# Kernel optimization log

Hardware: AMD Instinct MI355X
Metric: run time of the kernel (lower is better)

## Reference

```python
import jax, jax.numpy as jnp
import numpy as np
from jax import lax

N = 40       # num_users
K = 20       # num_channels
F = 3        # num_features (conv length dim)
SS = K * N   # state_size = 800
B = 16384


def _conv1d(x, w, b):
    # x: [B, C_in, L], w: [C_out, C_in, 3], SAME padding (pad=1)
    y = lax.conv_general_dilated(x, w, window_strides=(1,), padding=[(1, 1)],
                                 dimension_numbers=('NCH', 'OIH', 'NCH'))
    return y + b[None, :, None]


def _get_mask(state):
    # state: [B, SS, F]; status feature is index 2 (== -1 since F=3)
    visited = state[:, :, 2] != 0.0                      # [B, SS]
    vm = visited.reshape(B, K, N)                        # [B, K, N] (flat idx = chan*N + user)
    user_any = vm.any(axis=1)                            # [B, N]: user visited on any channel
    chan_full = vm.sum(axis=2) >= 2                      # [B, K]: channel has >=2 users
    mask = visited \
        | jnp.broadcast_to(user_any[:, None, :], (B, K, N)).reshape(B, SS) \
        | jnp.broadcast_to(chan_full[:, :, None], (B, K, N)).reshape(B, SS)
    return mask


def setup_inputs() -> dict:
    key = jax.random.key(0)
    ks = jax.random.split(key, 12)
    state = jax.random.normal(ks[0], (B, SS, F), jnp.float32)
    keep = jax.random.bernoulli(ks[1], 0.02, (B, SS)).astype(jnp.float32)
    state = state.at[:, :, 2].multiply(keep)
    s = 0.02
    w1 = jax.random.normal(ks[2], (128, SS, 3), jnp.float32) * s
    b1 = jnp.zeros((128,), jnp.float32)
    w2 = jax.random.normal(ks[3], (256, 128, 3), jnp.float32) * s
    b2 = jnp.zeros((256,), jnp.float32)
    w3 = jax.random.normal(ks[4], (128, 256, 3), jnp.float32) * s
    b3 = jnp.zeros((128,), jnp.float32)
    wl1 = jax.random.normal(ks[5], (64 * F, 128 * F), jnp.float32) * s   # [192, 384]
    bl1 = jnp.zeros((64 * F,), jnp.float32)
    wl2 = jax.random.normal(ks[6], (SS, 64 * F), jnp.float32) * s        # [800, 192]
    bl2 = jnp.zeros((SS,), jnp.float32)
    return {"state": state, "w1": w1, "b1": b1, "w2": w2, "b2": b2,
            "w3": w3, "b3": b3, "wl1": wl1, "bl1": bl1, "wl2": wl2, "bl2": bl2}


def reference(state, w1, b1, w2, b2, w3, b3, wl1, bl1, wl2, bl2):
    mask = _get_mask(state)
    x = jax.nn.relu(_conv1d(state, w1, b1))   # [B,128,3]
    x = jax.nn.relu(_conv1d(x, w2, b2))       # [B,256,3]
    x = jax.nn.relu(_conv1d(x, w3, b3))       # [B,128,3]
    x = x.reshape(B, -1)                      # [B,384]
    x = jax.nn.relu(x @ wl1.T + bl1)          # [B,192]
    out = x @ wl2.T + bl2                     # [B,800]
    return jnp.where(mask, -jnp.inf, out)
```

## Files before the change

kernel.cpp:

```cpp
#include <hip/hip_runtime.h>
#include <cstdint>
#include <cstddef>
#include <math.h>

typedef short bf16x8 __attribute__((ext_vector_type(8)));
typedef float f32x4 __attribute__((ext_vector_type(4)));
typedef unsigned long long u64;

#define NEG_HUGE (-3.0e38f)

__device__ __forceinline__ ushort f2bf(float x) {
    union { float f; uint32_t u; } a; a.f = x;
    uint32_t r = a.u + 0x7FFF + ((a.u >> 16) & 1);
    return (ushort)(r >> 16);
}

__device__ __forceinline__ void gload_lds16(const void* g, void* l) {
    __builtin_amdgcn_global_load_lds(
        (const __attribute__((address_space(1))) uint32_t*)g,
        (__attribute__((address_space(3))) uint32_t*)l, 16, 0, 0);
}

#define SCHED() __builtin_amdgcn_sched_barrier(0)
#define SBAR() do { SCHED(); __builtin_amdgcn_s_barrier(); SCHED(); } while (0)

__global__ void prep_conv_T(const float* __restrict__ w, ushort* __restrict__ WT,
                            int Cin, int Cout, int Nrows, int Kpad) {
    int idx = blockIdx.x * 256 + threadIdx.x;
    if (idx >= Nrows * Kpad) return;
    int n = idx / Kpad, k = idx - n * Kpad;
    float val = 0.f;
    if (k < Cin * 3) {
        int co = n / 3, l = n % 3, ci = k / 3, lx = k % 3;
        int t = lx - l + 1;
        if (t >= 0 && t < 3) val = w[(co * Cin + ci) * 3 + t];
    }
    WT[idx] = f2bf(val);
}

__global__ void prep_lin_T(const float* __restrict__ wl, ushort* __restrict__ WT,
                           int K, int Nreal, int Npad) {
    int idx = blockIdx.x * 256 + threadIdx.x;
    if (idx >= Npad * K) return;
    int n = idx / K, k = idx - n * K;
    WT[idx] = (n < Nreal) ? f2bf(wl[n * K + k]) : (ushort)0;
}

__global__ __launch_bounds__(512, 2)
void conv1_kernel(const float* __restrict__ state, const ushort* __restrict__ W1T,
                  const float* __restrict__ b1, ushort* __restrict__ X1g,
                  uint32_t* __restrict__ maskg)
{
    extern __shared__ char lds[];
    char* BF0 = lds;
    char* BF1 = lds + 8192;
    char* Wb0 = lds + 16384;
    char* Wb1 = lds + 65536;
    uint32_t* maskw = (uint32_t*)(lds + 114688);

    const int tid = threadIdx.x, lane = tid & 63, wid = tid >> 6;
    const int m0 = blockIdx.x * 64;
    const int ml = lane & 15, kq = lane >> 4;
    const int mbase = (wid >> 2) * 32;
    const int wn0 = (wid & 3) * 96;

    const int srow = tid >> 3, seg = tid & 7;
    const float* sbase = state + (size_t)(m0 + srow) * 2400 + seg * 8;

    f32x4 acc[6][2];
    #pragma unroll
    for (int f = 0; f < 6; ++f)
        #pragma unroll
        for (int mi = 0; mi < 2; ++mi) acc[f][mi] = (f32x4){0.f, 0.f, 0.f, 0.f};

    auto loadS = [&](float4 (&sv)[2], int c) {
        int kb = c * 64 + seg * 8;
        if (kb < 2400) {
            sv[0] = *(const float4*)(sbase + c * 64);
            sv[1] = *(const float4*)(sbase + c * 64 + 4);
        } else {
            sv[0] = (float4){0.f, 0.f, 0.f, 0.f};
            sv[1] = (float4){0.f, 0.f, 0.f, 0.f};
        }
    };
    auto stage_write = [&](float4 (&sv)[2], int c, char* dst) {
        float fv[8] = {sv[0].x, sv[0].y, sv[0].z, sv[0].w,
                       sv[1].x, sv[1].y, sv[1].z, sv[1].w};
        bf16x8 h;
        #pragma unroll
        for (int j = 0; j < 8; ++j) h[j] = (short)f2bf(fv[j]);
        *(bf16x8*)(dst + srow * 128 + ((seg * 16) ^ ((srow & 7) << 4))) = h;
        int kbase = c * 64 + seg * 8;
        int kmod = kbase % 3;
        uint32_t* mrow = &maskw[srow * 25];
        #define MCHK(J) { if (fv[J] != 0.0f) { int a = (kbase + (J)) / 3; \
                          atomicOr(&mrow[a >> 5], 1u << (a & 31)); } }
        if (kmod == 0)      { MCHK(2) MCHK(5) }
        else if (kmod == 1) { MCHK(1) MCHK(4) MCHK(7) }
        else                { MCHK(0) MCHK(3) MCHK(6) }
        #undef MCHK
    };
    auto loadW = [&](int c, char* dst) {
        #pragma unroll
        for (int i = 0; i < 6; ++i) {
            int s = i * 512 + tid;
            int r = s >> 3, o8 = s & 7;
            gload_lds16(W1T + (size_t)r * 2432 + c * 64 + ((o8 ^ (r & 7)) * 8),
                        dst + s * 16);
        }
    };
    auto mfmaC = [&](const char* wb, const char* sb) {
        #pragma unroll
        for (int ks = 0; ks < 2; ++ks) {
            bf16x8 af[6], bv[2];
            #pragma unroll
            for (int f = 0; f < 6; ++f) {
                int n = wn0 + f * 16 + ml;
                af[f] = *(const bf16x8*)(wb + n * 128 + (((ks * 4 + kq) * 16) ^ ((n & 7) << 4)));
            }
            #pragma unroll
            for (int mi = 0; mi < 2; ++mi) {
                int m = mbase + mi * 16 + ml;
                bv[mi] = *(const bf16x8*)(sb + m * 128 + (((ks * 4 + kq) * 16) ^ ((m & 7) << 4)));
            }
            #pragma unroll
            for (int f = 0; f < 6; ++f)
                #pragma unroll
                for (int mi = 0; mi < 2; ++mi)
                    acc[f][mi] = __builtin_amdgcn_mfma_f32_16x16x32_bf16(af[f], bv[mi], acc[f][mi], 0, 0, 0);
        }
    };

    for (int i = tid; i < 64 * 25; i += 512) maskw[i] = 0;
    float4 svA[2], svB[2];
    loadS(svA, 0);
    loadS(svB, 1);
    loadW(0, Wb0);
    asm volatile("s_waitcnt lgkmcnt(0)" ::: "memory");
    SBAR();

    #define BODY(SV, C, SB, WBC, WBN) do {                                   \
        stage_write(SV, (C), SB);                                            \
        loadS(SV, ((C) + 2 > 37) ? 37 : (C) + 2);                            \
        SCHED();                                                             \
        asm volatile("s_waitcnt lgkmcnt(0)" ::: "memory");                   \
        SBAR();                                                              \
        loadW(((C) + 1 > 37) ? 37 : (C) + 1, WBN);                           \
        SCHED();                                                             \
        asm volatile("s_waitcnt vmcnt(8)" ::: "memory");                     \
        SBAR();                                                              \
        mfmaC(WBC, SB);                                                      \
    } while (0)

    #pragma unroll 1
    for (int p = 0; p < 19; ++p) {
        BODY(svA, 2 * p,     BF0, Wb0, Wb1);
        BODY(svB, 2 * p + 1, BF1, Wb1, Wb0);
    }
    #undef BODY

    asm volatile("s_waitcnt vmcnt(0) lgkmcnt(0)" ::: "memory");
    SBAR();

    {
        const int nq4 = (lane >> 4) * 4;
        #pragma unroll
        for (int f = 0; f < 6; ++f) {
            int n4 = wn0 + f * 16 + nq4;
            float bv0 = b1[n4 / 3], bv1 = b1[(n4 + 1) / 3];
            float bv2 = b1[(n4 + 2) / 3], bv3 = b1[(n4 + 3) / 3];
            #pragma unroll
            for (int mi = 0; mi < 2; ++mi) {
                int m = mbase + mi * 16 + ml;
                ushort4 o;
                o.x = f2bf(fmaxf(acc[f][mi][0] + bv0, 0.f));
                o.y = f2bf(fmaxf(acc[f][mi][1] + bv1, 0.f));
                o.z = f2bf(fmaxf(acc[f][mi][2] + bv2, 0.f));
                o.w = f2bf(fmaxf(acc[f][mi][3] + bv3, 0.f));
                *(ushort4*)(X1g + (size_t)(m0 + m) * 384 + n4) = o;
            }
        }
    }

    if (tid < 64) {
        uint32_t* mw = &maskw[tid * 25];
        const u64 M40 = (1ull << 40) - 1;
        u64 ua = 0; uint32_t cf = 0;
        #pragma unroll
        for (int g = 0; g < 5; ++g) {
            uint32_t w0 = mw[5*g], w1 = mw[5*g+1], w2 = mw[5*g+2], w3 = mw[5*g+3], w4 = mw[5*g+4];
            u64 c0 = ( (u64)w0        | ((u64)w1 << 32)) & M40;
            u64 c1 = (((u64)w1 >> 8)  | ((u64)w2 << 24)) & M40;
            u64 c2 = (((u64)w2 >> 16) | ((u64)w3 << 16)) & M40;
            u64 c3 = (((u64)w3 >> 24) | ((u64)w4 << 8))  & M40;
            ua |= c0 | c1 | c2 | c3;
            if (__popcll(c0) >= 2) cf |= 1u << (4*g);
            if (__popcll(c1) >= 2) cf |= 1u << (4*g+1);
            if (__popcll(c2) >= 2) cf |= 1u << (4*g+2);
            if (__popcll(c3) >= 2) cf |= 1u << (4*g+3);
        }
        uint32_t* mg = maskg + (size_t)(m0 + tid) * 25;
        #pragma unroll
        for (int g = 0; g < 5; ++g) {
            uint32_t w0 = mw[5*g], w1 = mw[5*g+1], w2 = mw[5*g+2], w3 = mw[5*g+3], w4 = mw[5*g+4];
            u64 c0 = ( (u64)w0        | ((u64)w1 << 32)) & M40;
            u64 c1 = (((u64)w1 >> 8)  | ((u64)w2 << 24)) & M40;
            u64 c2 = (((u64)w2 >> 16) | ((u64)w3 << 16)) & M40;
            u64 c3 = (((u64)w3 >> 24) | ((u64)w4 << 8))  & M40;
            u64 m0v = c0 | ua | (((cf >> (4*g))     & 1u) ? M40 : 0ull);
            u64 m1v = c1 | ua | (((cf >> (4*g + 1)) & 1u) ? M40 : 0ull);
            u64 m2v = c2 | ua | (((cf >> (4*g + 2)) & 1u) ? M40 : 0ull);
            u64 m3v = c3 | ua | (((cf >> (4*g + 3)) & 1u) ? M40 : 0ull);
            mg[5*g]   = (uint32_t)m0v;
            mg[5*g+1] = (uint32_t)(m0v >> 32) | (uint32_t)(m1v << 8);
            mg[5*g+2] = (uint32_t)(m1v >> 24) | (uint32_t)(m2v << 16);
            mg[5*g+3] = (uint32_t)(m2v >> 16) | (uint32_t)(m3v << 24);
            mg[5*g+4] = (uint32_t)(m3v >> 8);
        }
    }
}

template<int K, bool BDIV3, bool RELU, bool F32OUT>
__global__ __launch_bounds__(512, 4)
void glayer3(const ushort* __restrict__ Ag, const ushort* __restrict__ WTg,
             const float* __restrict__ bias, void* __restrict__ Yg, int ldy,
             const uint32_t* __restrict__ maskg)
{
    constexpr int MF = 4, NF = 3;
    constexpr int MT = 128, NT = 192;
    constexpr int NC = K / 64;
    constexpr int ABYTES = MT * 128;
    constexpr int WBYTES = NT * 128;
    static_assert(NC >= 3, "pipeline assumes >=3 chunks");
    extern __shared__ char lds[];

    const int tid = threadIdx.x, lane = tid & 63, wid = tid >> 6;
    const int m0 = blockIdx.x * MT;
    const int n0 = blockIdx.y * NT;
    const int ml = lane & 15, kq = lane >> 4;
    const int mw = wid >> 2, nw = wid & 3;
    const int mbase = mw * MF * 16;
    const int wn0 = nw * NF * 16;

    f32x4 acc[NF][MF];
    #pragma unroll
    for (int f = 0; f < NF; ++f)
        #pragma unroll
        for (int mi = 0; mi < MF; ++mi) acc[f][mi] = (f32x4){0.f, 0.f, 0.f, 0.f};

    auto stage = [&](int c, int b) {
        char* Ab = lds + b * ABYTES;
        char* Wb = lds + 2 * ABYTES + b * WBYTES;
        #pragma unroll
        for (int i = 0; i < 2; ++i) {
            int s = i * 512 + tid;
            int r = s >> 3, o8 = s & 7;
            gload_lds16(Ag + (size_t)(m0 + r) * K + c * 64 + ((o8 ^ (r & 7)) * 8),
                        Ab + s * 16);
        }
        #pragma unroll
        for (int i = 0; i < 3; ++i) {
            int s = i * 512 + tid;
            int r = s >> 3, o8 = s & 7;
            gload_lds16(WTg + (size_t)(n0 + r) * K + c * 64 + ((o8 ^ (r & 7)) * 8),
                        Wb + s * 16);
        }
    };
    auto mfmaC = [&](int b) {
        const char* Ab = lds + b * ABYTES;
        const char* Wb = lds + 2 * ABYTES + b * WBYTES;
        #pragma unroll
        for (int ks = 0; ks < 2; ++ks) {
            bf16x8 af[NF], bv[MF];
            #pragma unroll
            for (int f = 0; f < NF; ++f) {
                int n = wn0 + f * 16 + ml;
                af[f] = *(const bf16x8*)(Wb + n * 128 + (((ks * 4 + kq) * 16) ^ ((n & 7) << 4)));
            }
            #pragma unroll
            for (int mi = 0; mi < MF; ++mi) {
                int m = mbase + mi * 16 + ml;
                bv[mi] = *(const bf16x8*)(Ab + m * 128 + (((ks * 4 + kq) * 16) ^ ((m & 7) << 4)));
            }
            #pragma unroll
            for (int f = 0; f < NF; ++f)
                #pragma unroll
                for (int mi = 0; mi < MF; ++mi)
                    acc[f][mi] = __builtin_amdgcn_mfma_f32_16x16x32_bf16(af[f], bv[mi], acc[f][mi], 0, 0, 0);
        }
    };

    stage(0, 0);
    stage(1, 1);
    asm volatile("s_waitcnt vmcnt(5)" ::: "memory");
    SBAR();

    #pragma unroll 1
    for (int c = 0; c < NC; ++c) {
        mfmaC(c & 1);
        if (c + 2 < NC) {
            SBAR();
            stage(c + 2, c & 1);
            asm volatile("s_waitcnt vmcnt(5)" ::: "memory");
            SBAR();
        } else if (c + 1 < NC) {
            SBAR();
            asm volatile("s_waitcnt vmcnt(0)" ::: "memory");
            SBAR();
        }
    }

    const int nq4 = (lane >> 4) * 4;
    if (!F32OUT) {
        ushort* Y = (ushort*)Yg;
        #pragma unroll
        for (int f = 0; f < NF; ++f) {
            int n4 = n0 + wn0 + f * 16 + nq4;
            float bv0 = bias[BDIV3 ? n4 / 3 : n4];
            float bv1 = bias[BDIV3 ? (n4 + 1) / 3 : n4 + 1];
            float bv2 = bias[BDIV3 ? (n4 + 2) / 3 : n4 + 2];
            float bv3 = bias[BDIV3 ? (n4 + 3) / 3 : n4 + 3];
            #pragma unroll
            for (int mi = 0; mi < MF; ++mi) {
                int m = mbase + mi * 16 + ml;
                float x0 = acc[f][mi][0] + bv0, x1 = acc[f][mi][1] + bv1;
                float x2 = acc[f][mi][2] + bv2, x3 = acc[f][mi][3] + bv3;
                if (RELU) { x0 = fmaxf(x0, 0.f); x1 = fmaxf(x1, 0.f);
                            x2 = fmaxf(x2, 0.f); x3 = fmaxf(x3, 0.f); }
                ushort4 o = {f2bf(x0), f2bf(x1), f2bf(x2), f2bf(x3)};
                *(ushort4*)(Y + (size_t)(m0 + m) * ldy + n4) = o;
            }
        }
    } else {
        float* Y = (float*)Yg;
        #pragma unroll
        for (int f = 0; f < NF; ++f) {
            int nf = n0 + wn0 + f * 16;
            if (nf < 800) {
                int n4 = nf + nq4, sh = n4 & 31;
                float bv0 = bias[n4], bv1 = bias[n4 + 1];
                float bv2 = bias[n4 + 2], bv3 = bias[n4 + 3];
                #pragma unroll
                for (int mi = 0; mi < MF; ++mi) {
                    int m = mbase + mi * 16 + ml;
                    uint32_t mwv = maskg[(size_t)(m0 + m) * 25 + (nf >> 5)];
                    float4 v;
                    v.x = ((mwv >> (sh + 0)) & 1u) ? NEG_HUGE : (acc[f][mi][0] + bv0);
                    v.y = ((mwv >> (sh + 1)) & 1u) ? NEG_HUGE : (acc[f][mi][1] + bv1);
                    v.z = ((mwv >> (sh + 2)) & 1u) ? NEG_HUGE : (acc[f][mi][2] + bv2);
                    v.w = ((mwv >> (sh + 3)) & 1u) ? NEG_HUGE : (acc[f][mi][3] + bv3);
                    *(float4*)(Y + (size_t)(m0 + m) * ldy + n4) = v;
                }
            }
        }
    }
}

__global__ void ws_fail_kernel(float* out) {
    if (threadIdx.x == 0 && blockIdx.x == 0) out[0] = NAN;
}

extern "C" void kernel_launch(void* const* d_in, const int* in_sizes, int n_in,
                              void* d_out, int out_size, void* d_ws, size_t ws_size,
                              hipStream_t stream) {
    const float* state = (const float*)d_in[0];
    const float* w1  = (const float*)d_in[1];
    const float* b1  = (const float*)d_in[2];
    const float* w2  = (const float*)d_in[3];
    const float* b2  = (const float*)d_in[4];
    const float* w3  = (const float*)d_in[5];
    const float* b3  = (const float*)d_in[6];
    const float* wl1 = (const float*)d_in[7];
    const float* bl1 = (const float*)d_in[8];
    const float* wl2 = (const float*)d_in[9];
    const float* bl2 = (const float*)d_in[10];
    float* out = (float*)d_out;

    char* ws = (char*)d_ws;
    size_t off = 0;
    auto carve = [&](size_t bytes) {
        char* p = ws + off;
        off = (off + bytes + 255) & ~(size_t)255;
        return p;
    };
    ushort* W1T  = (ushort*)carve(384ull * 2432 * 2);
    ushort* W2T  = (ushort*)carve(768ull * 384 * 2);
    ushort* W3T  = (ushort*)carve(384ull * 768 * 2);
    ushort* WL1T = (ushort*)carve(192ull * 384 * 2);
    ushort* WL2T = (ushort*)carve(960ull * 192 * 2);
    ushort* X1g  = (ushort*)carve(16384ull * 384 * 2);
    ushort* X2g  = (ushort*)carve(16384ull * 768 * 2);
    ushort* X3g  = (ushort*)carve(16384ull * 384 * 2);
    ushort* X4g  = (ushort*)carve(16384ull * 192 * 2);
    uint32_t* maskg = (uint32_t*)carve(16384ull * 25 * 4);

    if (off > ws_size) {
        ws_fail_kernel<<<1, 64, 0, stream>>>(out);
        return;
    }

    prep_conv_T<<<(384 * 2432 + 255) / 256, 256, 0, stream>>>(w1, W1T, 800, 128, 384, 2432);
    prep_conv_T<<<(768 * 384 + 255) / 256, 256, 0, stream>>>(w2, W2T, 128, 256, 768, 384);
    prep_conv_T<<<(384 * 768 + 255) / 256, 256, 0, stream>>>(w3, W3T, 256, 128, 384, 768);
    prep_lin_T<<<(192 * 384 + 255) / 256, 256, 0, stream>>>(wl1, WL1T, 384, 192, 192);
    prep_lin_T<<<(960 * 192 + 255) / 256, 256, 0, stream>>>(wl2, WL2T, 192, 800, 960);

    (void)hipFuncSetAttribute(reinterpret_cast<const void*>(conv1_kernel),
                        hipFuncAttributeMaxDynamicSharedMemorySize, 121088);
    conv1_kernel<<<256, 512, 121088, stream>>>(state, W1T, b1, X1g, maskg);

    auto kc2 = glayer3<384, true, true, false>;
    (void)hipFuncSetAttribute(reinterpret_cast<const void*>(kc2),
                        hipFuncAttributeMaxDynamicSharedMemorySize, 81920);
    kc2<<<dim3(128, 4), 512, 81920, stream>>>(X1g, W2T, b2, X2g, 768, nullptr);

    auto kc3 = glayer3<768, true, true, false>;
    (void)hipFuncSetAttribute(reinterpret_cast<const void*>(kc3),
                        hipFuncAttributeMaxDynamicSharedMemorySize, 81920);
    kc3<<<dim3(128, 2), 512, 81920, stream>>>(X2g, W3T, b3, X3g, 384, nullptr);

    auto kc4 = glayer3<384, false, true, false>;
    (void)hipFuncSetAttribute(reinterpret_cast<const void*>(kc4),
                        hipFuncAttributeMaxDynamicSharedMemorySize, 81920);
    kc4<<<dim3(128, 1), 512, 81920, stream>>>(X3g, WL1T, bl1, X4g, 192, nullptr);

    auto kc5 = glayer3<192, false, false, true>;
    (void)hipFuncSetAttribute(reinterpret_cast<const void*>(kc5),
                        hipFuncAttributeMaxDynamicSharedMemorySize, 81920);
    kc5<<<dim3(128, 5), 512, 81920, stream>>>(X4g, WL2T, bl2, out, 800, maskg);
}
```

Measured before the change: 149.4 us.

## Split conv1 output channels across two blocks and deepen state prefetch

Conv1 is launched with a 2D grid where each block computes half of the 384 output columns, halving per-block accumulators, weight tile LDS and MFMA work so that more blocks can be resident per CU. Only the first column-half block computes the action mask. The state prefetch is extended to three register buffers with adjusted waitcnt. The cost is that every state row is now loaded and converted twice, doubling global reads of the largest input unless caches absorb it.

```diff
diff --git a/kernel.cpp b/kernel.cpp
--- a/kernel.cpp
+++ b/kernel.cpp
@@ -46,7 +46,7 @@
     WT[idx] = (n < Nreal) ? f2bf(wl[n * K + k]) : (ushort)0;
 }
 
-__global__ __launch_bounds__(512, 2)
+__global__ __launch_bounds__(512, 4)
 void conv1_kernel(const float* __restrict__ state, const ushort* __restrict__ W1T,
                   const float* __restrict__ b1, ushort* __restrict__ X1g,
                   uint32_t* __restrict__ maskg)
@@ -55,21 +55,23 @@
     char* BF0 = lds;
     char* BF1 = lds + 8192;
     char* Wb0 = lds + 16384;
-    char* Wb1 = lds + 65536;
-    uint32_t* maskw = (uint32_t*)(lds + 114688);
+    char* Wb1 = lds + 40960;
+    uint32_t* maskw = (uint32_t*)(lds + 65536);
 
     const int tid = threadIdx.x, lane = tid & 63, wid = tid >> 6;
     const int m0 = blockIdx.x * 64;
+    const int n0 = blockIdx.y * 192;
+    const bool domask = (blockIdx.y == 0);
     const int ml = lane & 15, kq = lane >> 4;
     const int mbase = (wid >> 2) * 32;
-    const int wn0 = (wid & 3) * 96;
+    const int wn0 = (wid & 3) * 48;
 
     const int srow = tid >> 3, seg = tid & 7;
     const float* sbase = state + (size_t)(m0 + srow) * 2400 + seg * 8;
 
-    f32x4 acc[6][2];
+    f32x4 acc[3][2];
     #pragma unroll
-    for (int f = 0; f < 6; ++f)
+    for (int f = 0; f < 3; ++f)
         #pragma unroll
         for (int mi = 0; mi < 2; ++mi) acc[f][mi] = (f32x4){0.f, 0.f, 0.f, 0.f};
 
@@ -90,31 +92,33 @@
         #pragma unroll
         for (int j = 0; j < 8; ++j) h[j] = (short)f2bf(fv[j]);
         *(bf16x8*)(dst + srow * 128 + ((seg * 16) ^ ((srow & 7) << 4))) = h;
-        int kbase = c * 64 + seg * 8;
-        int kmod = kbase % 3;
-        uint32_t* mrow = &maskw[srow * 25];
-        #define MCHK(J) { if (fv[J] != 0.0f) { int a = (kbase + (J)) / 3; \
-                          atomicOr(&mrow[a >> 5], 1u << (a & 31)); } }
-        if (kmod == 0)      { MCHK(2) MCHK(5) }
-        else if (kmod == 1) { MCHK(1) MCHK(4) MCHK(7) }
-        else                { MCHK(0) MCHK(3) MCHK(6) }
-        #undef MCHK
+        if (domask) {
+            int kbase = c * 64 + seg * 8;
+            int kmod = kbase % 3;
+            uint32_t* mrow = &maskw[srow * 25];
+            #define MCHK(J) { if (fv[J] != 0.0f) { int a = (kbase + (J)) / 3; \
+                              atomicOr(&mrow[a >> 5], 1u << (a & 31)); } }
+            if (kmod == 0)      { MCHK(2) MCHK(5) }
+            else if (kmod == 1) { MCHK(1) MCHK(4) MCHK(7) }
+            else                { MCHK(0) MCHK(3) MCHK(6) }
+            #undef MCHK
+        }
     };
     auto loadW = [&](int c, char* dst) {
         #pragma unroll
-        for (int i = 0; i < 6; ++i) {
+        for (int i = 0; i < 3; ++i) {
             int s = i * 512 + tid;
             int r = s >> 3, o8 = s & 7;
-            gload_lds16(W1T + (size_t)r * 2432 + c * 64 + ((o8 ^ (r & 7)) * 8),
+            gload_lds16(W1T + (size_t)(n0 + r) * 2432 + c * 64 + ((o8 ^ (r & 7)) * 8),
                         dst + s * 16);
         }
     };
     auto mfmaC = [&](const char* wb, const char* sb) {
         #pragma unroll
         for (int ks = 0; ks < 2; ++ks) {
-            bf16x8 af[6], bv[2];
-            #pragma unroll
-            for (int f = 0; f < 6; ++f) {
+            bf16x8 af[3], bv[2];
+            #pragma unroll
+            for (int f = 0; f < 3; ++f) {
                 int n = wn0 + f * 16 + ml;
                 af[f] = *(const bf16x8*)(wb + n * 128 + (((ks * 4 + kq) * 16) ^ ((n & 7) << 4)));
             }
@@ -124,7 +128,7 @@
                 bv[mi] = *(const bf16x8*)(sb + m * 128 + (((ks * 4 + kq) * 16) ^ ((m & 7) << 4)));
             }
             #pragma unroll
-            for (int f = 0; f < 6; ++f)
+            for (int f = 0; f < 3; ++f)
                 #pragma unroll
                 for (int mi = 0; mi < 2; ++mi)
                     acc[f][mi] = __builtin_amdgcn_mfma_f32_16x16x32_bf16(af[f], bv[mi], acc[f][mi], 0, 0, 0);
@@ -132,31 +136,37 @@
     };
 
     for (int i = tid; i < 64 * 25; i += 512) maskw[i] = 0;
-    float4 svA[2], svB[2];
-    loadS(svA, 0);
-    loadS(svB, 1);
+    float4 sv0[2], sv1[2], sv2[2];
     loadW(0, Wb0);
-    asm volatile("s_waitcnt lgkmcnt(0)" ::: "memory");
+    loadS(sv0, 0);
+    loadS(sv1, 1);
+    loadS(sv2, 2);
+    SCHED();
+    asm volatile("s_waitcnt vmcnt(4) lgkmcnt(0)" ::: "memory");
     SBAR();
 
     #define BODY(SV, C, SB, WBC, WBN) do {                                   \
         stage_write(SV, (C), SB);                                            \
-        loadS(SV, ((C) + 2 > 37) ? 37 : (C) + 2);                            \
         SCHED();                                                             \
         asm volatile("s_waitcnt lgkmcnt(0)" ::: "memory");                   \
         SBAR();                                                              \
         loadW(((C) + 1 > 37) ? 37 : (C) + 1, WBN);                           \
+        loadS(SV, ((C) + 3 > 37) ? 37 : (C) + 3);                            \
         SCHED();                                                             \
-        asm volatile("s_waitcnt vmcnt(8)" ::: "memory");                     \
+        asm volatile("s_waitcnt vmcnt(7)" ::: "memory");                     \
         SBAR();                                                              \
         mfmaC(WBC, SB);                                                      \
     } while (0)
 
     #pragma unroll 1
-    for (int p = 0; p < 19; ++p) {
-        BODY(svA, 2 * p,     BF0, Wb0, Wb1);
-        BODY(svB, 2 * p + 1, BF1, Wb1, Wb0);
-    }
+    for (int p = 0; p < 12; ++p) {
+        int c = 3 * p;
+        BODY(sv0, c,     (c & 1) ? BF1 : BF0, (c & 1) ? Wb1 : Wb0, (c & 1) ? Wb0 : Wb1);
+        BODY(sv1, c + 1, ((c + 1) & 1) ? BF1 : BF0, ((c + 1) & 1) ? Wb1 : Wb0, ((c + 1) & 1) ? Wb0 : Wb1);
+        BODY(sv2, c + 2, ((c + 2) & 1) ? BF1 : BF0, ((c + 2) & 1) ? Wb1 : Wb0, ((c + 2) & 1) ? Wb0 : Wb1);
+    }
+    BODY(sv0, 36, BF0, Wb0, Wb1);
+    BODY(sv1, 37, BF1, Wb1, Wb0);
     #undef BODY
 
     asm volatile("s_waitcnt vmcnt(0) lgkmcnt(0)" ::: "memory");
@@ -165,8 +175,8 @@
     {
         const int nq4 = (lane >> 4) * 4;
         #pragma unroll
-        for (int f = 0; f < 6; ++f) {
-            int n4 = wn0 + f * 16 + nq4;
+        for (int f = 0; f < 3; ++f) {
+            int n4 = n0 + wn0 + f * 16 + nq4;
             float bv0 = b1[n4 / 3], bv1 = b1[(n4 + 1) / 3];
             float bv2 = b1[(n4 + 2) / 3], bv3 = b1[(n4 + 3) / 3];
             #pragma unroll
@@ -182,7 +192,7 @@
         }
     }
 
-    if (tid < 64) {
+    if (domask && tid < 64) {
         uint32_t* mw = &maskw[tid * 25];
         const u64 M40 = (1ull << 40) - 1;
         u64 ua = 0; uint32_t cf = 0;
@@ -406,8 +416,8 @@
     prep_lin_T<<<(960 * 192 + 255) / 256, 256, 0, stream>>>(wl2, WL2T, 192, 800, 960);
 
     (void)hipFuncSetAttribute(reinterpret_cast<const void*>(conv1_kernel),
-                        hipFuncAttributeMaxDynamicSharedMemorySize, 121088);
-    conv1_kernel<<<256, 512, 121088, stream>>>(state, W1T, b1, X1g, maskg);
+                        hipFuncAttributeMaxDynamicSharedMemorySize, 71936);
+    conv1_kernel<<<dim3(256, 2), 512, 71936, stream>>>(state, W1T, b1, X1g, maskg);
 
     auto kc2 = glayer3<384, true, true, false>;
     (void)hipFuncSetAttribute(reinterpret_cast<const void*>(kc2),
```

After: 170.9 us. 14.4% more time.
